# Kernel optimization log

Measured on AMD Instinct MI355X. Metric: run time of the kernel, lower is better.

## Reference

```python
import jax, jax.numpy as jnp
import numpy as np
from jax import lax

A = 9                 # 3 ratios x 3 scales
STRIDE = 16
PRE_NMS = 6000
POST_NMS = 300
NMS_THRESH = 0.7
POOL = 7
SAMPLES = 2           # roi-align sampling ratio
N_CLASSES = 21


def _generate_anchors(base=16.0, ratios=(0.5, 1.0, 2.0), scales=(8.0, 16.0, 32.0)):
    ratios = np.asarray(ratios, np.float64)
    scales = np.asarray(scales, np.float64)
    ctr = (base - 1.0) / 2.0
    size = base * base
    ws = np.round(np.sqrt(size / ratios))
    hs = np.round(ws * ratios)
    out = []
    for w0, h0 in zip(ws, hs):
        w2 = w0 * scales
        h2 = h0 * scales
        out.append(np.stack([ctr - (w2 - 1) / 2, ctr - (h2 - 1) / 2,
                             ctr + (w2 - 1) / 2, ctr + (h2 - 1) / 2], 1))
    return np.concatenate(out, 0).astype(np.float32)  # [A,4]


def _decode(anchors, deltas):
    # bbox_transform_inv with +1 width/height convention
    w = anchors[:, 2] - anchors[:, 0] + 1.0
    h = anchors[:, 3] - anchors[:, 1] + 1.0
    cx = anchors[:, 0] + 0.5 * w
    cy = anchors[:, 1] + 0.5 * h
    pcx = deltas[:, 0] * w + cx
    pcy = deltas[:, 1] * h + cy
    pw = jnp.exp(deltas[:, 2]) * w
    ph = jnp.exp(deltas[:, 3]) * h
    return jnp.stack([pcx - 0.5 * pw, pcy - 0.5 * ph,
                      pcx + 0.5 * pw, pcy + 0.5 * ph], 1)


def _nms_keep(boxes, thresh):
    # greedy NMS over score-sorted boxes; precomputed [N,N] IoU (memory-bound)
    N = boxes.shape[0]
    x1, y1, x2, y2 = boxes[:, 0], boxes[:, 1], boxes[:, 2], boxes[:, 3]
    areas = (x2 - x1 + 1.0) * (y2 - y1 + 1.0)
    xx1 = jnp.maximum(x1[:, None], x1[None, :])
    yy1 = jnp.maximum(y1[:, None], y1[None, :])
    xx2 = jnp.minimum(x2[:, None], x2[None, :])
    yy2 = jnp.minimum(y2[:, None], y2[None, :])
    inter = jnp.maximum(xx2 - xx1 + 1.0, 0.0) * jnp.maximum(yy2 - yy1 + 1.0, 0.0)
    iou = inter / (areas[:, None] + areas[None, :] - inter)
    ridx = jnp.arange(N)
    def body(i, supp):
        return supp | ((iou[i] > thresh) & (ridx > i) & ~supp[i])
    supp = lax.fori_loop(0, N, body, jnp.zeros((N,), bool))
    return ~supp


def _roi_align(feat, boxes, scale, out, ratio):
    # feat [C,H,W], boxes [R,4] in image coords -> [R,C,out,out]
    C, H, W = feat.shape
    R = boxes.shape[0]
    S = out * ratio
    x1 = boxes[:, 0] * scale
    y1 = boxes[:, 1] * scale
    x2 = boxes[:, 2] * scale
    y2 = boxes[:, 3] * scale
    bw = jnp.maximum(x2 - x1, 1.0) / out
    bh = jnp.maximum(y2 - y1, 1.0) / out
    off = (jnp.arange(S, dtype=feat.dtype) + 0.5) / ratio
    xs = jnp.clip(x1[:, None] + off[None, :] * bw[:, None], 0.0, W - 1.0)  # [R,S]
    ys = jnp.clip(y1[:, None] + off[None, :] * bh[:, None], 0.0, H - 1.0)
    x0 = jnp.floor(xs); y0 = jnp.floor(ys)
    lx = xs - x0; ly = ys - y0
    x0i = x0.astype(jnp.int32); x1i = jnp.minimum(x0i + 1, W - 1)
    y0i = y0.astype(jnp.int32); y1i = jnp.minimum(y0i + 1, H - 1)
    def g(yi, xi):  # gather -> [C,R,S,S]
        return feat[:, yi[:, :, None], xi[:, None, :]]
    wy0 = (1.0 - ly)[:, :, None]; wy1 = ly[:, :, None]
    wx0 = (1.0 - lx)[:, None, :]; wx1 = lx[:, None, :]
    val = (g(y0i, x0i) * (wy0 * wx0) + g(y0i, x1i) * (wy0 * wx1)
           + g(y1i, x0i) * (wy1 * wx0) + g(y1i, x1i) * (wy1 * wx1))
    pooled = val.reshape(C, R, out, ratio, out, ratio).mean(axis=(3, 5))
    return pooled.transpose(1, 0, 2, 3)


def setup_inputs() -> dict:
    key = jax.random.key(0)
    ks = jax.random.split(key, 8)
    base_feat = jax.random.normal(ks[0], (1, 1024, 64, 100), jnp.float32) * 0.5
    im_info = jnp.array([[1024.0, 1600.0, 1.0]], jnp.float32)  # H, W, scale
    rpn_conv_w = jax.random.normal(ks[1], (512, 1024, 3, 3), jnp.float32) * 0.01
    rpn_conv_b = jnp.zeros((512,), jnp.float32)
    rpn_cls_w = jax.random.normal(ks[2], (2 * A, 512), jnp.float32) * 0.01
    rpn_cls_b = jnp.zeros((2 * A,), jnp.float32)
    rpn_bbox_w = jax.random.normal(ks[3], (4 * A, 512), jnp.float32) * 0.01
    rpn_bbox_b = jnp.zeros((4 * A,), jnp.float32)
    fc_w = jax.random.normal(ks[4], (1024, 2048), jnp.float32) * 0.02
    fc_b = jnp.zeros((2048,), jnp.float32)
    cls_w = jax.random.normal(ks[5], (2048, N_CLASSES), jnp.float32) * 0.02
    cls_b = jnp.zeros((N_CLASSES,), jnp.float32)
    bbox_w = jax.random.normal(ks[6], (2048, 4 * N_CLASSES), jnp.float32) * 0.02
    bbox_b = jnp.zeros((4 * N_CLASSES,), jnp.float32)
    return dict(base_feat=base_feat, im_info=im_info,
                rpn_conv_w=rpn_conv_w, rpn_conv_b=rpn_conv_b,
                rpn_cls_w=rpn_cls_w, rpn_cls_b=rpn_cls_b,
                rpn_bbox_w=rpn_bbox_w, rpn_bbox_b=rpn_bbox_b,
                fc_w=fc_w, fc_b=fc_b, cls_w=cls_w, cls_b=cls_b,
                bbox_w=bbox_w, bbox_b=bbox_b)


def reference(base_feat, im_info, rpn_conv_w, rpn_conv_b, rpn_cls_w, rpn_cls_b,
              rpn_bbox_w, rpn_bbox_b, fc_w, fc_b, cls_w, cls_b, bbox_w, bbox_b):
    _, C, Hf, Wf = base_feat.shape
    # --- RPN head ---
    h = lax.conv_general_dilated(base_feat, rpn_conv_w, (1, 1), 'SAME',
                                 dimension_numbers=('NCHW', 'OIHW', 'NCHW'))
    h = jax.nn.relu(h + rpn_conv_b[None, :, None, None])
    cls_logits = jnp.einsum('nchw,oc->nohw', h, rpn_cls_w) + rpn_cls_b[None, :, None, None]
    bbox_out = jnp.einsum('nchw,oc->nohw', h, rpn_bbox_w) + rpn_bbox_b[None, :, None, None]
    # fg prob: channels are [bg(A), fg(A)] -> softmax over 2
    fg = jax.nn.softmax(cls_logits[0].reshape(2, A, Hf, Wf), axis=0)[1]  # [A,H,W]
    scores = fg.transpose(1, 2, 0).reshape(-1)                 # (H*W*A,)
    deltas = bbox_out[0].transpose(1, 2, 0).reshape(-1, 4)     # (H*W*A,4)
    # --- proposal layer ---
    anchors = jnp.asarray(_generate_anchors())
    sx = jnp.arange(Wf, dtype=jnp.float32) * STRIDE
    sy = jnp.arange(Hf, dtype=jnp.float32) * STRIDE
    gx, gy = jnp.meshgrid(sx, sy)                              # [H,W]
    shifts = jnp.stack([gx, gy, gx, gy], -1).reshape(-1, 4)    # [H*W,4]
    all_anchors = (shifts[:, None, :] + anchors[None, :, :]).reshape(-1, 4)
    boxes = _decode(all_anchors, deltas)
    im_h = im_info[0, 0]; im_w = im_info[0, 1]
    boxes = jnp.stack([jnp.clip(boxes[:, 0], 0.0, im_w - 1.0),
                       jnp.clip(boxes[:, 1], 0.0, im_h - 1.0),
                       jnp.clip(boxes[:, 2], 0.0, im_w - 1.0),
                       jnp.clip(boxes[:, 3], 0.0, im_h - 1.0)], 1)
    _, order = lax.top_k(scores, PRE_NMS)
    boxes_top = boxes[order]                                   # score-sorted desc
    keep = _nms_keep(boxes_top, NMS_THRESH)
    prio = keep.astype(jnp.float32) * (PRE_NMS - jnp.arange(PRE_NMS, dtype=jnp.float32))
    _, sel = lax.top_k(prio, POST_NMS)
    valid = keep[sel]
    roi_boxes = jnp.where(valid[:, None], boxes_top[sel], 0.0)  # zero-pad like original
    rois = jnp.concatenate([jnp.zeros((POST_NMS, 1), roi_boxes.dtype), roi_boxes], 1)
    # --- RoIAlign + head (proposals detached, as in the original) ---
    pooled = _roi_align(base_feat[0], lax.stop_gradient(roi_boxes), 1.0 / STRIDE, POOL, SAMPLES)
    vec = pooled.mean(axis=(2, 3))                             # [R,1024]
    hidden = jax.nn.relu(vec @ fc_w + fc_b)
    cls_prob = jax.nn.softmax(hidden @ cls_w + cls_b, axis=-1)
    bbox_pred = hidden @ bbox_w + bbox_b
    return rois, cls_prob, bbox_pred
```

## Files before the change

### kernel.cpp

```cpp
#include <hip/hip_runtime.h>


#define OFF_CLS   26214400u
#define OFF_BBOX  26675200u
#define OFF_BOXES 27596800u
#define OFF_KEYS  28518400u
#define OFF_HIST  28979200u
#define OFF_META  29241344u
#define OFF_RNK   29241600u
#define OFF_CAND  29472000u
#define OFF_BTOP  29702400u
#define OFF_MASK  29798400u
#define OFF_ROIB  34310400u
#define OFF_VEC   34315200u
#define OFF_HID   35544000u

__global__ __launch_bounds__(64) void k_conv(const float* __restrict__ in,
                                             const float* __restrict__ wgt,
                                             const float* __restrict__ bias,
                                             float* __restrict__ out) {
  const int lane = threadIdx.x;
  const int pg = blockIdx.x * 64 + lane;
  const int p0 = pg * 4;
  const int y  = p0 / 100;
  const int x0 = p0 % 100;
  const int ocb = blockIdx.y * 8;

  __shared__ float sw[288 * 8];

  float acc[8][4];
#pragma unroll
  for (int j = 0; j < 8; ++j)
#pragma unroll
    for (int q = 0; q < 4; ++q) acc[j][q] = 0.f;

  const bool vr_[3] = { (y - 1) >= 0, true, (y + 1) < 64 };
  const bool le = (x0 > 0), re = (x0 + 4 < 100);

  float bufA[3][6], bufB[3][6];

#define LOADIC(R, IC)                                                          \
  {                                                                            \
    const float* pin = in + (size_t)(IC) * 6400;                               \
    _Pragma("unroll")                                                          \
    for (int dy = 0; dy < 3; ++dy) {                                           \
      const int yy = y + dy - 1;                                               \
      const bool vr = vr_[dy];                                                 \
      const float* prow = pin + yy * 100;                                      \
      float4 m = vr ? *(const float4*)(prow + x0)                              \
                    : make_float4(0.f, 0.f, 0.f, 0.f);                         \
      R[dy][1] = m.x; R[dy][2] = m.y; R[dy][3] = m.z; R[dy][4] = m.w;          \
      R[dy][0] = (vr && le) ? prow[x0 - 1] : 0.f;                              \
      R[dy][5] = (vr && re) ? prow[x0 + 4] : 0.f;                              \
    }                                                                          \
  }

#define TAPS(R, ICL)                                                           \
  {                                                                            \
    _Pragma("unroll")                                                          \
    for (int tap = 0; tap < 9; ++tap) {                                        \
      const int dy = tap / 3, kx = tap % 3;                                    \
      const float* swp = &sw[((ICL) * 9 + tap) * 8];                           \
      float4 w0 = *(const float4*)(swp);                                       \
      float4 w1 = *(const float4*)(swp + 4);                                   \
      float wv[8] = {w0.x, w0.y, w0.z, w0.w, w1.x, w1.y, w1.z, w1.w};          \
      _Pragma("unroll")                                                        \
      for (int j = 0; j < 8; ++j)                                              \
        _Pragma("unroll")                                                      \
        for (int q = 0; q < 4; ++q)                                            \
          acc[j][q] = fmaf(R[dy][q + kx], wv[j], acc[j][q]);                   \
    }                                                                          \
  }

  LOADIC(bufA, 0);

  for (int icb = 0; icb < 1024; icb += 32) {
    __syncthreads();
#pragma unroll
    for (int k = lane; k < 576; k += 64) {
      const int ocl = k / 72, r4 = k % 72;
      float4 v = *(const float4*)(wgt + (size_t)(ocb + ocl) * 9216 + icb * 9 + r4 * 4);
      sw[(r4 * 4 + 0) * 8 + ocl] = v.x;
      sw[(r4 * 4 + 1) * 8 + ocl] = v.y;
      sw[(r4 * 4 + 2) * 8 + ocl] = v.z;
      sw[(r4 * 4 + 3) * 8 + ocl] = v.w;
    }
    __syncthreads();

    for (int icl = 0; icl < 32; icl += 2) {
      const int ic = icb + icl;
      LOADIC(bufB, ic + 1);
      TAPS(bufA, icl);
      if (ic + 2 < 1024) LOADIC(bufA, ic + 2);
      TAPS(bufB, icl + 1);
    }
  }

#pragma unroll
  for (int j = 0; j < 8; ++j) {
    const int oc = ocb + j;
    const float b = bias[oc];
    float4 o;
    o.x = fmaxf(acc[j][0] + b, 0.f);
    o.y = fmaxf(acc[j][1] + b, 0.f);
    o.z = fmaxf(acc[j][2] + b, 0.f);
    o.w = fmaxf(acc[j][3] + b, 0.f);
    *(float4*)(out + (size_t)oc * 6400 + p0) = o;
  }
#undef LOADIC
#undef TAPS
}

__global__ __launch_bounds__(256) void k_rpn(const float* __restrict__ h,
                                             const float* __restrict__ cls_w,
                                             const float* __restrict__ cls_b,
                                             const float* __restrict__ bbox_w,
                                             const float* __restrict__ bbox_b,
                                             float* __restrict__ cls_out,
                                             float* __restrict__ bbox_out) {
  __shared__ float swt[64 * 56 + 16];
  const int tx = threadIdx.x, ty = threadIdx.y;
  const int tid = ty * 64 + tx;
  const int px = blockIdx.x * 64 + tx;

  float acc[16];
#pragma unroll
  for (int j = 0; j < 16; ++j) acc[j] = 0.f;

  for (int cb = 0; cb < 512; cb += 64) {
    __syncthreads();
    for (int k = tid; k < 64 * 54; k += 256) {
      int o = k / 64, cl = k % 64;
      swt[cl * 56 + o] = (o < 18) ? cls_w[o * 512 + cb + cl]
                                  : bbox_w[(o - 18) * 512 + cb + cl];
    }
    __syncthreads();
    for (int cl = 0; cl < 64; ++cl) {
      float hv = h[(size_t)(cb + cl) * 6400 + px];
      const float* wp = swt + cl * 56 + ty * 16;
      float4 w0 = *(const float4*)(wp);
      float4 w1 = *(const float4*)(wp + 4);
      float4 w2 = *(const float4*)(wp + 8);
      float4 w3 = *(const float4*)(wp + 12);
      acc[0]  = fmaf(hv, w0.x, acc[0]);  acc[1]  = fmaf(hv, w0.y, acc[1]);
      acc[2]  = fmaf(hv, w0.z, acc[2]);  acc[3]  = fmaf(hv, w0.w, acc[3]);
      acc[4]  = fmaf(hv, w1.x, acc[4]);  acc[5]  = fmaf(hv, w1.y, acc[5]);
      acc[6]  = fmaf(hv, w1.z, acc[6]);  acc[7]  = fmaf(hv, w1.w, acc[7]);
      acc[8]  = fmaf(hv, w2.x, acc[8]);  acc[9]  = fmaf(hv, w2.y, acc[9]);
      acc[10] = fmaf(hv, w2.z, acc[10]); acc[11] = fmaf(hv, w2.w, acc[11]);
      acc[12] = fmaf(hv, w3.x, acc[12]); acc[13] = fmaf(hv, w3.y, acc[13]);
      acc[14] = fmaf(hv, w3.z, acc[14]); acc[15] = fmaf(hv, w3.w, acc[15]);
    }
  }
#pragma unroll
  for (int j = 0; j < 16; ++j) {
    int o = ty * 16 + j;
    if (o < 54) {
      float v = acc[j] + ((o < 18) ? cls_b[o] : bbox_b[o - 18]);
      if (o < 18) cls_out[(size_t)o * 6400 + px] = v;
      else        bbox_out[(size_t)(o - 18) * 6400 + px] = v;
    }
  }
}

__global__ __launch_bounds__(256) void k_transpose(const float* __restrict__ in,
                                                   float* __restrict__ outp) {
  __shared__ float tile[64][65];
  const int tx = threadIdx.x, ty = threadIdx.y;
  const int cb = blockIdx.x * 64, pb = blockIdx.y * 64;
  for (int rr = ty; rr < 64; rr += 4)
    tile[rr][tx] = in[(size_t)(cb + rr) * 6400 + pb + tx];
  __syncthreads();
  for (int rr = ty; rr < 64; rr += 4)
    outp[(size_t)(pb + rr) * 1024 + cb + tx] = tile[tx][rr];
}

__global__ __launch_bounds__(256) void k_score(const float* __restrict__ cls,
                                               const float* __restrict__ bbx,
                                               const float* __restrict__ im_info,
                                               float4* __restrict__ boxes,
                                               unsigned long long* __restrict__ keys,
                                               unsigned int* __restrict__ hist) {
  const int i = blockIdx.x * 256 + threadIdx.x;
  if (i >= 57600) return;
  const int p = i / 9, a = i % 9;
  const int yy = p / 100, xx = p % 100;

  const float anc[9][4] = {
    {-84.f,-40.f,99.f,55.f},   {-176.f,-88.f,191.f,103.f}, {-360.f,-184.f,375.f,199.f},
    {-56.f,-56.f,71.f,71.f},   {-120.f,-120.f,135.f,135.f},{-248.f,-248.f,263.f,263.f},
    {-36.f,-80.f,51.f,95.f},   {-80.f,-168.f,95.f,183.f},  {-168.f,-344.f,183.f,359.f}};

  float l0 = cls[(size_t)a * 6400 + p];
  float l1 = cls[(size_t)(9 + a) * 6400 + p];
  float mx = fmaxf(l0, l1);
  float e0 = expf(l0 - mx), e1 = expf(l1 - mx);
  float sc = e1 / (e0 + e1);

  float d0 = bbx[(size_t)(4 * a + 0) * 6400 + p];
  float d1 = bbx[(size_t)(4 * a + 1) * 6400 + p];
  float d2 = bbx[(size_t)(4 * a + 2) * 6400 + p];
  float d3 = bbx[(size_t)(4 * a + 3) * 6400 + p];

  float ax1 = anc[a][0] + xx * 16.f, ay1 = anc[a][1] + yy * 16.f;
  float ax2 = anc[a][2] + xx * 16.f, ay2 = anc[a][3] + yy * 16.f;
  float w = ax2 - ax1 + 1.f, hh = ay2 - ay1 + 1.f;
  float cx = ax1 + 0.5f * w, cy = ay1 + 0.5f * hh;
  float pcx = d0 * w + cx, pcy = d1 * hh + cy;
  float pw = expf(d2) * w, ph = expf(d3) * hh;
  float bx1 = pcx - 0.5f * pw, by1 = pcy - 0.5f * ph;
  float bx2 = pcx + 0.5f * pw, by2 = pcy + 0.5f * ph;

  float imh = im_info[0], imw = im_info[1];
  bx1 = fminf(fmaxf(bx1, 0.f), imw - 1.f);
  by1 = fminf(fmaxf(by1, 0.f), imh - 1.f);
  bx2 = fminf(fmaxf(bx2, 0.f), imw - 1.f);
  by2 = fminf(fmaxf(by2, 0.f), imh - 1.f);

  boxes[i] = make_float4(bx1, by1, bx2, by2);
  unsigned sb = __float_as_uint(sc);
  keys[i] = ((unsigned long long)sb << 32) | (unsigned long long)(0xFFFFFFFFu - (unsigned)i);
  atomicAdd(&hist[sb >> 16], 1u);
}

__global__ __launch_bounds__(256) void k_cutoff(const unsigned int* __restrict__ hist,
                                                unsigned int* __restrict__ meta) {
  __shared__ unsigned csum[256];
  __shared__ unsigned sbin[256];
  __shared__ int schunk;
  __shared__ unsigned sacc;
  const int t = threadIdx.x;
  unsigned s = 0;
  for (int b = 0; b < 256; ++b) s += hist[t * 256 + b];
  csum[t] = s;
  __syncthreads();
  if (t == 0) {
    unsigned acc = 0; int tc = 0;
    for (int c = 255; c >= 0; --c) {
      if (acc + csum[c] >= 6000u) { tc = c; break; }
      acc += csum[c];
    }
    schunk = tc; sacc = acc;
  }
  __syncthreads();
  const int tc = schunk;
  sbin[t] = hist[tc * 256 + t];
  __syncthreads();
  if (t == 0) {
    unsigned acc = sacc; int bstar = tc * 256;
    for (int b = 255; b >= 0; --b) {
      acc += sbin[b];
      if (acc >= 6000u) { bstar = tc * 256 + b; break; }
    }
    meta[0] = (unsigned)bstar;
  }
}

__global__ __launch_bounds__(256) void k_compact(const unsigned long long* __restrict__ keys,
                                                 unsigned int* __restrict__ meta,
                                                 int* __restrict__ cand) {
  const int i = blockIdx.x * 256 + threadIdx.x;
  if (i >= 57600) return;
  unsigned bin = (unsigned)(keys[i] >> 48);
  if (bin >= meta[0]) {
    unsigned pos = atomicAdd(&meta[1], 1u);
    cand[pos] = i;
  }
}

__global__ __launch_bounds__(256) void k_rank(const unsigned long long* __restrict__ keys,
                                              const unsigned int* __restrict__ meta,
                                              const int* __restrict__ cand,
                                              int* __restrict__ rnk) {
  __shared__ unsigned long long sk[256];
  const int nc = (int)meta[1];
  if (blockIdx.x * 256 >= nc) return;
  const int cs = blockIdx.x * 256 + threadIdx.x;
  const bool act = cs < nc;
  const unsigned long long mk = act ? keys[cand[cs]] : ~0ull;
  int cnt = 0;
  const int base = blockIdx.y * 7200;
  for (int cb = 0; cb < 7200; cb += 256) {
    sk[threadIdx.x] = (cb + threadIdx.x < 7200) ? keys[base + cb + threadIdx.x] : 0ull;
    __syncthreads();
    if (act) {
#pragma unroll 8
      for (int j = 0; j < 256; ++j) cnt += (sk[j] > mk) ? 1 : 0;
    }
    __syncthreads();
  }
  if (act && cnt) atomicAdd(&rnk[cs], cnt);
}

__global__ __launch_bounds__(256) void k_scatter(const float4* __restrict__ boxes,
                                                 const unsigned int* __restrict__ meta,
                                                 const int* __restrict__ cand,
                                                 const int* __restrict__ rnk,
                                                 float4* __restrict__ btop) {
  const int cs = blockIdx.x * 256 + threadIdx.x;
  if (cs < (int)meta[1]) {
    int r = rnk[cs];
    if (r < 6000) btop[r] = boxes[cand[cs]];
  }
}

__global__ __launch_bounds__(256) void k_mask(const float4* __restrict__ btop,
                                              unsigned long long* __restrict__ mask) {
  const int lane = threadIdx.x;
  const int i = blockIdx.y * 4 + threadIdx.y;
  const int w = blockIdx.x;
  const int j = w * 64 + lane;
  float4 bi = btop[i];
  float4 bj = (j < 6000) ? btop[j] : make_float4(0.f, 0.f, 0.f, 0.f);
  float ai = (bi.z - bi.x + 1.f) * (bi.w - bi.y + 1.f);
  float aj = (bj.z - bj.x + 1.f) * (bj.w - bj.y + 1.f);
  float xx1 = fmaxf(bi.x, bj.x), yy1 = fmaxf(bi.y, bj.y);
  float xx2 = fminf(bi.z, bj.z), yy2 = fminf(bi.w, bj.w);
  float inter = fmaxf(xx2 - xx1 + 1.f, 0.f) * fmaxf(yy2 - yy1 + 1.f, 0.f);
  float iou = inter / (ai + aj - inter);
  bool sup = (j < 6000) && (j > i) && (iou > 0.7f);
  unsigned long long bal = __ballot(sup);
  if (lane == 0) mask[(size_t)i * 94 + w] = bal;
}

__global__ __launch_bounds__(64) void k_nms_scan(const unsigned long long* __restrict__ mask,
                                                 const float4* __restrict__ btop,
                                                 float4* __restrict__ roib,
                                                 float* __restrict__ rois) {
  const int lane = threadIdx.x;
  for (int k = lane; k < 1500; k += 64) rois[k] = 0.f;
  {
    float4 z = make_float4(0.f, 0.f, 0.f, 0.f);
    for (int k = lane; k < 300; k += 64) roib[k] = z;
  }
  unsigned long long sLo = 0ull, sHi = 0ull;
  unsigned long long pLo[8], pHi[8];
  float4 pBx[8];
#pragma unroll
  for (int u = 0; u < 8; ++u) {
    pLo[u] = mask[(size_t)u * 94 + lane];
    pHi[u] = (lane < 30) ? mask[(size_t)u * 94 + 64 + lane] : 0ull;
    pBx[u] = btop[u];
  }
  int kc = 0;
  for (int base = 0; base < 6000; base += 8) {
#pragma unroll
    for (int u = 0; u < 8; ++u) {
      const int i = base + u;
      unsigned long long rowLo = pLo[u], rowHi = pHi[u];
      float4 bx = pBx[u];
      const int ip = i + 8;
      if (ip < 6000) {
        pLo[u] = mask[(size_t)ip * 94 + lane];
        pHi[u] = (lane < 30) ? mask[(size_t)ip * 94 + 64 + lane] : 0ull;
        pBx[u] = btop[ip];
      }
      const int w = i >> 6, b = i & 63;
      unsigned long long cw = (w < 64) ? __shfl(sLo, w, 64) : __shfl(sHi, w - 64, 64);
      if (!((cw >> b) & 1ull)) {
        if (lane == 0) {
          rois[kc * 5 + 1] = bx.x; rois[kc * 5 + 2] = bx.y;
          rois[kc * 5 + 3] = bx.z; rois[kc * 5 + 4] = bx.w;
          roib[kc] = bx;
        }
        sLo |= rowLo;
        if (lane < 30) sHi |= rowHi;
        ++kc;
        if (kc >= 300) return;
      }
    }
  }
}

__global__ __launch_bounds__(256) void k_roialign(const float* __restrict__ ft,
                                                  const float4* __restrict__ roib,
                                                  float* __restrict__ vec) {
  const int r = blockIdx.x;
  const int tid = threadIdx.x;
  __shared__ int sx0[14], sx1[14], sy0[14], sy1[14];
  __shared__ float slx[14], sly[14];

  float4 bx = roib[r];
  float x1 = bx.x * 0.0625f, y1 = bx.y * 0.0625f;
  float x2 = bx.z * 0.0625f, y2 = bx.w * 0.0625f;
  float bw = fmaxf(x2 - x1, 1.0f) / 7.0f;
  float bh = fmaxf(y2 - y1, 1.0f) / 7.0f;
  if (tid < 14) {
    float off = ((float)tid + 0.5f) / 2.0f;
    float xs = fminf(fmaxf(x1 + off * bw, 0.f), 99.f);
    float x0f = floorf(xs);
    sx0[tid] = (int)x0f;
    sx1[tid] = min((int)x0f + 1, 99);
    slx[tid] = xs - x0f;
  } else if (tid < 28) {
    int t = tid - 14;
    float off = ((float)t + 0.5f) / 2.0f;
    float ys = fminf(fmaxf(y1 + off * bh, 0.f), 63.f);
    float y0f = floorf(ys);
    sy0[t] = (int)y0f;
    sy1[t] = min((int)y0f + 1, 63);
    sly[t] = ys - y0f;
  }
  __syncthreads();

  float ax = 0.f, ay = 0.f, az = 0.f, aw = 0.f;
  for (int py = 0; py < 7; ++py) {
    for (int px = 0; px < 7; ++px) {
      float cx_ = 0.f, cy_ = 0.f, cz_ = 0.f, cw_ = 0.f;
#pragma unroll
      for (int ss = 0; ss < 2; ++ss) {
        const int s = py * 2 + ss;
        const int yA = sy0[s], yB = sy1[s];
        const float ly = sly[s];
#pragma unroll
        for (int tt = 0; tt < 2; ++tt) {
          const int t = px * 2 + tt;
          const int xA = sx0[t], xB = sx1[t];
          const float lx = slx[t];
          const float w00 = (1.f - ly) * (1.f - lx), w01 = (1.f - ly) * lx;
          const float w10 = ly * (1.f - lx),         w11 = ly * lx;
          const float4 v00 = *(const float4*)(ft + ((size_t)(yA * 100 + xA) << 10) + (tid << 2));
          const float4 v01 = *(const float4*)(ft + ((size_t)(yA * 100 + xB) << 10) + (tid << 2));
          const float4 v10 = *(const float4*)(ft + ((size_t)(yB * 100 + xA) << 10) + (tid << 2));
          const float4 v11 = *(const float4*)(ft + ((size_t)(yB * 100 + xB) << 10) + (tid << 2));
          cx_ += v00.x * w00 + v01.x * w01 + v10.x * w10 + v11.x * w11;
          cy_ += v00.y * w00 + v01.y * w01 + v10.y * w10 + v11.y * w11;
          cz_ += v00.z * w00 + v01.z * w01 + v10.z * w10 + v11.z * w11;
          cw_ += v00.w * w00 + v01.w * w01 + v10.w * w10 + v11.w * w11;
        }
      }
      ax += cx_ * 0.25f; ay += cy_ * 0.25f; az += cz_ * 0.25f; aw += cw_ * 0.25f;
    }
  }
  float4 o;
  o.x = ax / 49.0f; o.y = ay / 49.0f; o.z = az / 49.0f; o.w = aw / 49.0f;
  *(float4*)(vec + (size_t)r * 1024 + (tid << 2)) = o;
}

__global__ __launch_bounds__(256) void k_fc1(const float* __restrict__ vec,
                                             const float* __restrict__ fw,
                                             const float* __restrict__ fb,
                                             float* __restrict__ hidden) {
  __shared__ float sa[12][1024];
  const int tx = threadIdx.x, ty = threadIdx.y;
  const int tid = ty * 64 + tx;
  const int nb = blockIdx.x * 256, mb = blockIdx.y * 12;

  for (int mm = 0; mm < 12; ++mm) {
    int m = mb + mm;
    float4 v = (m < 300) ? ((const float4*)(vec + (size_t)m * 1024))[tid]
                         : make_float4(0.f, 0.f, 0.f, 0.f);
    ((float4*)sa[mm])[tid] = v;
  }
  __syncthreads();

  const int n = nb + tx * 4;
  float acc[3][4];
#pragma unroll
  for (int mi = 0; mi < 3; ++mi)
#pragma unroll
    for (int q = 0; q < 4; ++q) acc[mi][q] = 0.f;

  for (int k = 0; k < 1024; ++k) {
    float4 b4 = *(const float4*)(fw + (size_t)k * 2048 + n);
#pragma unroll
    for (int mi = 0; mi < 3; ++mi) {
      float a = sa[ty * 3 + mi][k];
      acc[mi][0] = fmaf(a, b4.x, acc[mi][0]);
      acc[mi][1] = fmaf(a, b4.y, acc[mi][1]);
      acc[mi][2] = fmaf(a, b4.z, acc[mi][2]);
      acc[mi][3] = fmaf(a, b4.w, acc[mi][3]);
    }
  }
  float4 bias = *(const float4*)(fb + n);
#pragma unroll
  for (int mi = 0; mi < 3; ++mi) {
    int m = mb + ty * 3 + mi;
    if (m < 300) {
      float4 o;
      o.x = fmaxf(acc[mi][0] + bias.x, 0.f);
      o.y = fmaxf(acc[mi][1] + bias.y, 0.f);
      o.z = fmaxf(acc[mi][2] + bias.z, 0.f);
      o.w = fmaxf(acc[mi][3] + bias.w, 0.f);
      *(float4*)(hidden + (size_t)m * 2048 + n) = o;
    }
  }
}

__global__ __launch_bounds__(128) void k_head(const float* __restrict__ hidden,
                                              const float* __restrict__ cw,
                                              const float* __restrict__ cbias,
                                              const float* __restrict__ bw,
                                              const float* __restrict__ bbias,
                                              float* __restrict__ out_cls,
                                              float* __restrict__ out_bbox) {
  const int m = blockIdx.x, tid = threadIdx.x;
  __shared__ float sh[2048];
  __shared__ float slog[32];
  __shared__ float sred[2];
  for (int k = tid; k < 512; k += 128)
    ((float4*)sh)[k] = ((const float4*)(hidden + (size_t)m * 2048))[k];
  __syncthreads();
  if (tid < 21) {
    float a = 0.f;
#pragma unroll 4
    for (int k = 0; k < 2048; ++k) a = fmaf(sh[k], cw[(size_t)k * 21 + tid], a);
    slog[tid] = a + cbias[tid];
  } else if (tid < 105) {
    int j = tid - 21;
    float a = 0.f;
#pragma unroll 4
    for (int k = 0; k < 2048; ++k) a = fmaf(sh[k], bw[(size_t)k * 84 + j], a);
    out_bbox[(size_t)m * 84 + j] = a + bbias[j];
  }
  __syncthreads();
  if (tid == 0) {
    float mx = slog[0];
    for (int o = 1; o < 21; ++o) mx = fmaxf(mx, slog[o]);
    float sm = 0.f;
    for (int o = 0; o < 21; ++o) sm += expf(slog[o] - mx);
    sred[0] = mx; sred[1] = sm;
  }
  __syncthreads();
  if (tid < 21) out_cls[(size_t)m * 21 + tid] = expf(slog[tid] - sred[0]) / sred[1];
}

extern "C" void kernel_launch(void* const* d_in, const int* in_sizes, int n_in,
                              void* d_out, int out_size, void* d_ws, size_t ws_size,
                              hipStream_t stream) {
  const float* base_feat  = (const float*)d_in[0];
  const float* im_info    = (const float*)d_in[1];
  const float* rpn_conv_w = (const float*)d_in[2];
  const float* rpn_conv_b = (const float*)d_in[3];
  const float* rpn_cls_w  = (const float*)d_in[4];
  const float* rpn_cls_b  = (const float*)d_in[5];
  const float* rpn_bbox_w = (const float*)d_in[6];
  const float* rpn_bbox_b = (const float*)d_in[7];
  const float* fc_w   = (const float*)d_in[8];
  const float* fc_b   = (const float*)d_in[9];
  const float* cls_w  = (const float*)d_in[10];
  const float* cls_b  = (const float*)d_in[11];
  const float* bbox_w = (const float*)d_in[12];
  const float* bbox_b = (const float*)d_in[13];

  char* ws = (char*)d_ws;
  float* h     = (float*)(ws);
  float* ft    = (float*)(ws);
  float* clsL  = (float*)(ws + OFF_CLS);
  float* bboxL = (float*)(ws + OFF_BBOX);
  float4* boxes4 = (float4*)(ws + OFF_BOXES);
  unsigned long long* keys = (unsigned long long*)(ws + OFF_KEYS);
  unsigned int* hist = (unsigned int*)(ws + OFF_HIST);
  unsigned int* meta = (unsigned int*)(ws + OFF_META);
  int* rnk  = (int*)(ws + OFF_RNK);
  int* cand = (int*)(ws + OFF_CAND);
  float4* btop4 = (float4*)(ws + OFF_BTOP);
  unsigned long long* mask = (unsigned long long*)(ws + OFF_MASK);
  float4* roib4 = (float4*)(ws + OFF_ROIB);
  float* vec    = (float*)(ws + OFF_VEC);
  float* hidden = (float*)(ws + OFF_HID);

  float* out = (float*)d_out;

  hipMemsetAsync(ws + OFF_HIST, 0, 262144u + 256u + 230400u, stream);

  k_conv<<<dim3(25, 64), dim3(64), 0, stream>>>(base_feat, rpn_conv_w, rpn_conv_b, h);
  k_rpn<<<dim3(100), dim3(64, 4), 0, stream>>>(h, rpn_cls_w, rpn_cls_b, rpn_bbox_w, rpn_bbox_b,
                                               clsL, bboxL);
  k_transpose<<<dim3(16, 100), dim3(64, 4), 0, stream>>>(base_feat, ft);
  k_score<<<dim3(225), dim3(256), 0, stream>>>(clsL, bboxL, im_info, boxes4, keys, hist);
  k_cutoff<<<dim3(1), dim3(256), 0, stream>>>(hist, meta);
  k_compact<<<dim3(225), dim3(256), 0, stream>>>(keys, meta, cand);
  k_rank<<<dim3(225, 8), dim3(256), 0, stream>>>(keys, meta, cand, rnk);
  k_scatter<<<dim3(225), dim3(256), 0, stream>>>(boxes4, meta, cand, rnk, btop4);
  k_mask<<<dim3(94, 1500), dim3(64, 4), 0, stream>>>(btop4, mask);
  k_nms_scan<<<dim3(1), dim3(64), 0, stream>>>(mask, btop4, roib4, out);
  k_roialign<<<dim3(300), dim3(256), 0, stream>>>(ft, roib4, vec);
  k_fc1<<<dim3(8, 25), dim3(64, 4), 0, stream>>>(vec, fc_w, fc_b, hidden);
  k_head<<<dim3(300), dim3(128), 0, stream>>>(hidden, cls_w, cls_b, bbox_w, bbox_b,
                                              out + 1500, out + 7800);
}
```

Before: 2.307 ms.

## Pre-transpose conv weights, software-pipeline weight row loads, batch NMS mask rows

Adds a kernel that transposes the RPN conv weights once into an oc-group-major layout. The conv can then stage each 32-channel block with plain contiguous float4 copies instead of scattered strided shared-memory writes. Weight rows are double-buffered in registers between shared memory and the FMAs, which should hide LDS latency behind the inner loop at the cost of extra registers and an extra launch. Separately, the NMS mask kernel processes 8 rows per thread to reuse the column box and cut the grid size, and the memset is moved later in the stream.

```diff
diff --git a/kernel.cpp b/kernel.cpp
--- a/kernel.cpp
+++ b/kernel.cpp
@@ -1,6 +1,7 @@
 #include <hip/hip_runtime.h>
 
 
+#define OFF_WT    13107200u
 #define OFF_CLS   26214400u
 #define OFF_BBOX  26675200u
 #define OFF_BOXES 27596800u
@@ -15,8 +16,35 @@
 #define OFF_VEC   34315200u
 #define OFF_HID   35544000u
 
+__global__ __launch_bounds__(256) void k_wtr(const float* __restrict__ wgt,
+                                             float* __restrict__ wT) {
+  __shared__ float tile[8][513];
+  const int g = blockIdx.x;
+  const int rt = blockIdx.y;
+  const int tid = threadIdx.x;
+
+  for (int v = tid; v < 1024; v += 256) {
+    const int ocl = v >> 7, c4 = v & 127;
+    float4 m = *(const float4*)(wgt + (size_t)(g * 8 + ocl) * 9216 + rt * 512 + c4 * 4);
+    tile[ocl][c4 * 4 + 0] = m.x;
+    tile[ocl][c4 * 4 + 1] = m.y;
+    tile[ocl][c4 * 4 + 2] = m.z;
+    tile[ocl][c4 * 4 + 3] = m.w;
+  }
+  __syncthreads();
+  float* dst = wT + (size_t)g * 73728 + (size_t)rt * 4096;
+  for (int o4 = tid; o4 < 1024; o4 += 256) {
+    float4 m;
+    m.x = tile[(4 * o4 + 0) & 7][(4 * o4 + 0) >> 3];
+    m.y = tile[(4 * o4 + 1) & 7][(4 * o4 + 1) >> 3];
+    m.z = tile[(4 * o4 + 2) & 7][(4 * o4 + 2) >> 3];
+    m.w = tile[(4 * o4 + 3) & 7][(4 * o4 + 3) >> 3];
+    *(float4*)(dst + 4 * o4) = m;
+  }
+}
+
 __global__ __launch_bounds__(64) void k_conv(const float* __restrict__ in,
-                                             const float* __restrict__ wgt,
+                                             const float* __restrict__ wT,
                                              const float* __restrict__ bias,
                                              float* __restrict__ out) {
   const int lane = threadIdx.x;
@@ -24,9 +52,10 @@
   const int p0 = pg * 4;
   const int y  = p0 / 100;
   const int x0 = p0 % 100;
-  const int ocb = blockIdx.y * 8;
-
-  __shared__ float sw[288 * 8];
+  const int g  = blockIdx.y;
+  const int ocb = g * 8;
+
+  __shared__ __align__(16) float sw2[2304];
 
   float acc[8][4];
 #pragma unroll
@@ -34,65 +63,101 @@
 #pragma unroll
     for (int q = 0; q < 4; ++q) acc[j][q] = 0.f;
 
-  const bool vr_[3] = { (y - 1) >= 0, true, (y + 1) < 64 };
+  const bool vr0 = (y - 1) >= 0;
+  const bool vr2 = (y + 1) < 64;
   const bool le = (x0 > 0), re = (x0 + 4 < 100);
 
   float bufA[3][6], bufB[3][6];
+  float wA[24], wB[24];
 
 #define LOADIC(R, IC)                                                          \
   {                                                                            \
     const float* pin = in + (size_t)(IC) * 6400;                               \
+    {                                                                          \
+      const float* p_ = pin + (y - 1) * 100;                                   \
+      float4 m = vr0 ? *(const float4*)(p_ + x0)                               \
+                     : make_float4(0.f, 0.f, 0.f, 0.f);                        \
+      R[0][1] = m.x; R[0][2] = m.y; R[0][3] = m.z; R[0][4] = m.w;              \
+      R[0][0] = (vr0 && le) ? p_[x0 - 1] : 0.f;                                \
+      R[0][5] = (vr0 && re) ? p_[x0 + 4] : 0.f;                                \
+    }                                                                          \
+    {                                                                          \
+      const float* p_ = pin + y * 100;                                         \
+      float4 m = *(const float4*)(p_ + x0);                                    \
+      R[1][1] = m.x; R[1][2] = m.y; R[1][3] = m.z; R[1][4] = m.w;              \
+      R[1][0] = le ? p_[x0 - 1] : 0.f;                                         \
+      R[1][5] = re ? p_[x0 + 4] : 0.f;                                         \
+    }                                                                          \
+    {                                                                          \
+      const float* p_ = pin + (y + 1) * 100;                                   \
+      float4 m = vr2 ? *(const float4*)(p_ + x0)                               \
+                     : make_float4(0.f, 0.f, 0.f, 0.f);                        \
+      R[2][1] = m.x; R[2][2] = m.y; R[2][3] = m.z; R[2][4] = m.w;              \
+      R[2][0] = (vr2 && le) ? p_[x0 - 1] : 0.f;                                \
+      R[2][5] = (vr2 && re) ? p_[x0 + 4] : 0.f;                                \
+    }                                                                          \
+  }
+
+#define LOADROW(W, ICL, DY)                                                    \
+  {                                                                            \
+    const float4* wp = (const float4*)&sw2[(ICL) * 72 + (DY) * 24];            \
     _Pragma("unroll")                                                          \
-    for (int dy = 0; dy < 3; ++dy) {                                           \
-      const int yy = y + dy - 1;                                               \
-      const bool vr = vr_[dy];                                                 \
-      const float* prow = pin + yy * 100;                                      \
-      float4 m = vr ? *(const float4*)(prow + x0)                              \
-                    : make_float4(0.f, 0.f, 0.f, 0.f);                         \
-      R[dy][1] = m.x; R[dy][2] = m.y; R[dy][3] = m.z; R[dy][4] = m.w;          \
-      R[dy][0] = (vr && le) ? prow[x0 - 1] : 0.f;                              \
-      R[dy][5] = (vr && re) ? prow[x0 + 4] : 0.f;                              \
+    for (int t4 = 0; t4 < 6; ++t4) {                                           \
+      float4 v = wp[t4];                                                       \
+      W[t4 * 4 + 0] = v.x; W[t4 * 4 + 1] = v.y;                                \
+      W[t4 * 4 + 2] = v.z; W[t4 * 4 + 3] = v.w;                                \
     }                                                                          \
   }
 
-#define TAPS(R, ICL)                                                           \
+#define ROWFMA(R, DY, W)                                                       \
   {                                                                            \
     _Pragma("unroll")                                                          \
-    for (int tap = 0; tap < 9; ++tap) {                                        \
-      const int dy = tap / 3, kx = tap % 3;                                    \
-      const float* swp = &sw[((ICL) * 9 + tap) * 8];                           \
-      float4 w0 = *(const float4*)(swp);                                       \
-      float4 w1 = *(const float4*)(swp + 4);                                   \
-      float wv[8] = {w0.x, w0.y, w0.z, w0.w, w1.x, w1.y, w1.z, w1.w};          \
+    for (int kx = 0; kx < 3; ++kx) {                                           \
       _Pragma("unroll")                                                        \
-      for (int j = 0; j < 8; ++j)                                              \
+      for (int j = 0; j < 8; ++j) {                                            \
+        const float wv = W[kx * 8 + j];                                        \
         _Pragma("unroll")                                                      \
         for (int q = 0; q < 4; ++q)                                            \
-          acc[j][q] = fmaf(R[dy][q + kx], wv[j], acc[j][q]);                   \
+          acc[j][q] = fmaf(R[DY][q + kx], wv, acc[j][q]);                      \
+      }                                                                        \
     }                                                                          \
   }
 
+#define STAGE(ICB)                                                             \
+  {                                                                            \
+    const float* gsrc = wT + (size_t)g * 73728 + (size_t)(ICB) * 72;           \
+    _Pragma("unroll")                                                          \
+    for (int s = 0; s < 9; ++s) {                                              \
+      float4 v = *(const float4*)(gsrc + (size_t)(lane + 64 * s) * 4);         \
+      ((float4*)sw2)[lane + 64 * s] = v;                                       \
+    }                                                                          \
+  }
+
+  STAGE(0);
   LOADIC(bufA, 0);
+  __syncthreads();
+  LOADROW(wA, 0, 0);
 
   for (int icb = 0; icb < 1024; icb += 32) {
-    __syncthreads();
-#pragma unroll
-    for (int k = lane; k < 576; k += 64) {
-      const int ocl = k / 72, r4 = k % 72;
-      float4 v = *(const float4*)(wgt + (size_t)(ocb + ocl) * 9216 + icb * 9 + r4 * 4);
-      sw[(r4 * 4 + 0) * 8 + ocl] = v.x;
-      sw[(r4 * 4 + 1) * 8 + ocl] = v.y;
-      sw[(r4 * 4 + 2) * 8 + ocl] = v.z;
-      sw[(r4 * 4 + 3) * 8 + ocl] = v.w;
-    }
-    __syncthreads();
-
     for (int icl = 0; icl < 32; icl += 2) {
       const int ic = icb + icl;
       LOADIC(bufB, ic + 1);
-      TAPS(bufA, icl);
+      LOADROW(wB, icl, 1);      ROWFMA(bufA, 0, wA);
+      LOADROW(wA, icl, 2);      ROWFMA(bufA, 1, wB);
+      LOADROW(wB, icl + 1, 0);  ROWFMA(bufA, 2, wA);
       if (ic + 2 < 1024) LOADIC(bufA, ic + 2);
-      TAPS(bufB, icl + 1);
+      LOADROW(wA, icl + 1, 1);  ROWFMA(bufB, 0, wB);
+      LOADROW(wB, icl + 1, 2);  ROWFMA(bufB, 1, wA);
+      if (icl + 2 < 32) {
+        LOADROW(wA, icl + 2, 0);
+      }
+      ROWFMA(bufB, 2, wB);
+    }
+    if (icb + 32 < 1024) {
+      __syncthreads();
+      STAGE(icb + 32);
+      __syncthreads();
+      LOADROW(wA, 0, 0);
     }
   }
 
@@ -108,7 +173,9 @@
     *(float4*)(out + (size_t)oc * 6400 + p0) = o;
   }
 #undef LOADIC
-#undef TAPS
+#undef LOADROW
+#undef ROWFMA
+#undef STAGE
 }
 
 __global__ __launch_bounds__(256) void k_rpn(const float* __restrict__ h,
@@ -307,20 +374,26 @@
 __global__ __launch_bounds__(256) void k_mask(const float4* __restrict__ btop,
                                               unsigned long long* __restrict__ mask) {
   const int lane = threadIdx.x;
-  const int i = blockIdx.y * 4 + threadIdx.y;
   const int w = blockIdx.x;
   const int j = w * 64 + lane;
-  float4 bi = btop[i];
+  const int ibase = blockIdx.y * 32 + threadIdx.y * 8;
   float4 bj = (j < 6000) ? btop[j] : make_float4(0.f, 0.f, 0.f, 0.f);
-  float ai = (bi.z - bi.x + 1.f) * (bi.w - bi.y + 1.f);
   float aj = (bj.z - bj.x + 1.f) * (bj.w - bj.y + 1.f);
-  float xx1 = fmaxf(bi.x, bj.x), yy1 = fmaxf(bi.y, bj.y);
-  float xx2 = fminf(bi.z, bj.z), yy2 = fminf(bi.w, bj.w);
-  float inter = fmaxf(xx2 - xx1 + 1.f, 0.f) * fmaxf(yy2 - yy1 + 1.f, 0.f);
-  float iou = inter / (ai + aj - inter);
-  bool sup = (j < 6000) && (j > i) && (iou > 0.7f);
-  unsigned long long bal = __ballot(sup);
-  if (lane == 0) mask[(size_t)i * 94 + w] = bal;
+#pragma unroll
+  for (int u = 0; u < 8; ++u) {
+    const int i = ibase + u;
+    if (i < 6000) {
+      float4 bi = btop[i];
+      float ai = (bi.z - bi.x + 1.f) * (bi.w - bi.y + 1.f);
+      float xx1 = fmaxf(bi.x, bj.x), yy1 = fmaxf(bi.y, bj.y);
+      float xx2 = fminf(bi.z, bj.z), yy2 = fminf(bi.w, bj.w);
+      float inter = fmaxf(xx2 - xx1 + 1.f, 0.f) * fmaxf(yy2 - yy1 + 1.f, 0.f);
+      float iou = inter / (ai + aj - inter);
+      bool sup = (j < 6000) && (j > i) && (iou > 0.7f);
+      unsigned long long bal = __ballot(sup);
+      if (lane == 0) mask[(size_t)i * 94 + w] = bal;
+    }
+  }
 }
 
 __global__ __launch_bounds__(64) void k_nms_scan(const unsigned long long* __restrict__ mask,
@@ -546,6 +619,7 @@
   char* ws = (char*)d_ws;
   float* h     = (float*)(ws);
   float* ft    = (float*)(ws);
+  float* wT    = (float*)(ws + OFF_WT);
   float* clsL  = (float*)(ws + OFF_CLS);
   float* bboxL = (float*)(ws + OFF_BBOX);
   float4* boxes4 = (float4*)(ws + OFF_BOXES);
@@ -562,18 +636,18 @@
 
   float* out = (float*)d_out;
 
-  hipMemsetAsync(ws + OFF_HIST, 0, 262144u + 256u + 230400u, stream);
-
-  k_conv<<<dim3(25, 64), dim3(64), 0, stream>>>(base_feat, rpn_conv_w, rpn_conv_b, h);
+  k_wtr<<<dim3(64, 18), dim3(256), 0, stream>>>(rpn_conv_w, wT);
+  k_conv<<<dim3(25, 64), dim3(64), 0, stream>>>(base_feat, wT, rpn_conv_b, h);
   k_rpn<<<dim3(100), dim3(64, 4), 0, stream>>>(h, rpn_cls_w, rpn_cls_b, rpn_bbox_w, rpn_bbox_b,
                                                clsL, bboxL);
+  hipMemsetAsync(ws + OFF_HIST, 0, 262144u + 256u + 230400u, stream);
   k_transpose<<<dim3(16, 100), dim3(64, 4), 0, stream>>>(base_feat, ft);
   k_score<<<dim3(225), dim3(256), 0, stream>>>(clsL, bboxL, im_info, boxes4, keys, hist);
   k_cutoff<<<dim3(1), dim3(256), 0, stream>>>(hist, meta);
   k_compact<<<dim3(225), dim3(256), 0, stream>>>(keys, meta, cand);
   k_rank<<<dim3(225, 8), dim3(256), 0, stream>>>(keys, meta, cand, rnk);
   k_scatter<<<dim3(225), dim3(256), 0, stream>>>(boxes4, meta, cand, rnk, btop4);
-  k_mask<<<dim3(94, 1500), dim3(64, 4), 0, stream>>>(btop4, mask);
+  k_mask<<<dim3(94, 188), dim3(64, 4), 0, stream>>>(btop4, mask);
   k_nms_scan<<<dim3(1), dim3(64), 0, stream>>>(mask, btop4, roib4, out);
   k_roialign<<<dim3(300), dim3(256), 0, stream>>>(ft, roib4, vec);
   k_fc1<<<dim3(8, 25), dim3(64, 4), 0, stream>>>(vec, fc_w, fc_b, hidden);
```

Result: slower. 3.400 ms (+47.3%).
